# Optimization experiments

Hardware: AMD Instinct MI355X
Metric: run time of the kernel (lower is better)

The kernel has to match this reference:

```python
import jax, jax.numpy as jnp
import numpy as np

KERNEL_SIZE = 6
PAD = (KERNEL_SIZE - 2) // 4  # 1


def _polyphase(k1d):
    # torch: flip(k.reshape(-1,2).permute(1,0), dims=(1,)) -> (2, K/2)
    # row 0 = even-index taps reversed, row 1 = odd-index taps reversed
    return jnp.flip(k1d.reshape(-1, 2).T, axis=1)


def _upfir_last(x, f):
    """Polyphase synthesis along last axis.
    x: (..., N), f: (2, K2). Pads reflect by PAD, correlates with each
    polyphase filter (stride-1 cross-correlation as in F.conv2d), then
    interleaves the two outputs -> (..., 2N). Even outputs come from f[0].
    """
    N = x.shape[-1]
    K2 = f.shape[1]
    pad_cfg = [(0, 0)] * (x.ndim - 1) + [(PAD, PAD)]
    xp = jnp.pad(x, pad_cfg, mode='reflect')  # (..., N + 2*PAD), N+2*PAD-K2+1 == N
    y0 = sum(f[0, j] * xp[..., j:j + N] for j in range(K2))
    y1 = sum(f[1, j] * xp[..., j:j + N] for j in range(K2))
    return jnp.stack([y0, y1], axis=-1).reshape(*x.shape[:-1], 2 * N)


def _upfir_rows(x, f):
    # synthesis along axis -2 (the H axis); matches torch's .mT transpose dance
    return jnp.swapaxes(_upfir_last(jnp.swapaxes(x, -1, -2), f), -1, -2)


def setup_inputs() -> dict:
    key = jax.random.key(0)
    ks = jax.random.split(key, 6)
    B, C, H, W = 4, 64, 256, 256
    return {
        'ss': jax.random.normal(ks[0], (B, C, H, W), dtype=jnp.float32),
        'sd': jax.random.normal(ks[1], (B, C, H, W), dtype=jnp.float32),
        'ds': jax.random.normal(ks[2], (B, C, H, W), dtype=jnp.float32),
        'dd': jax.random.normal(ks[3], (B, C, H, W), dtype=jnp.float32),
        'h': jax.random.normal(ks[4], (KERNEL_SIZE,), dtype=jnp.float32),
        'g': jax.random.normal(ks[5], (KERNEL_SIZE,), dtype=jnp.float32),
    }


def reference(ss, sd, ds, dd, h, g):
    # single level inverse 2D DWT (levels=1, normalize_approximation=False)
    fh = _polyphase(h)
    fg = _polyphase(g)
    # columns pass (along H): reconstruct low-pass rows `s` and high-pass rows `d`
    s = _upfir_rows(ss, fh) + _upfir_rows(sd, fg)  # (B,C,2H,W)
    d = _upfir_rows(ds, fh) + _upfir_rows(dd, fg)  # (B,C,2H,W)
    # rows pass (along W)
    out = _upfir_last(s, fh) + _upfir_last(d, fg)  # (B,C,2H,2W)
    return out
```

## Files before the change

### kernel.cpp

```cpp
#include <hip/hip_runtime.h>


typedef float float4v __attribute__((ext_vector_type(4)));

constexpr int Hc = 256;
constexpr int Wc = 256;
constexpr int ROWS = 8;
constexpr int WPB  = 4;

__global__ __launch_bounds__(256) void idwt_kernel(
    const float* __restrict__ ss, const float* __restrict__ sd,
    const float* __restrict__ ds, const float* __restrict__ dd,
    const float* __restrict__ hf, const float* __restrict__ gf,
    float* __restrict__ out)
{
    const int lane = threadIdx.x;
    const int wid  = threadIdx.y;
    const int i0   = (blockIdx.x * WPB + wid) * ROWS;
    const int bc   = blockIdx.y;

    const float h0 = hf[0], h1 = hf[1], h2 = hf[2];
    const float h3 = hf[3], h4 = hf[4], h5 = hf[5];
    const float g0 = gf[0], g1 = gf[1], g2 = gf[2];
    const float g3 = gf[3], g4 = gf[4], g5 = gf[5];

    const size_t off = (size_t)bc * (Hc * Wc);
    const int j0 = lane * 4;
    const float* pss = ss + off + j0;
    const float* psd = sd + off + j0;
    const float* pds = ds + off + j0;
    const float* pdd = dd + off + j0;

    auto ld = [&](const float* p, int r) -> float4v {
        return *reinterpret_cast<const float4v*>(p + (size_t)r * Wc);
    };

    const int rm = (i0 == 0) ? 1 : i0 - 1;
    float4v s_m = ld(pss, rm), s_c = ld(pss, i0);
    float4v t_m = ld(psd, rm), t_c = ld(psd, i0);
    float4v u_m = ld(pds, rm), u_c = ld(pds, i0);
    float4v v_m = ld(pdd, rm), v_c = ld(pdd, i0);

    const int W2 = 2 * Wc;
    float* obase = out + (size_t)bc * (2 * Hc) * W2 + 8 * lane;

    auto left = [&](const float4v& w) -> float {
        float l = __shfl_up(w[3], 1);
        return (lane == 0) ? w[1] : l;
    };
    auto right = [&](const float4v& w) -> float {
        float rr = __shfl_down(w[0], 1);
        return (lane == 63) ? w[2] : rr;
    };

    #pragma unroll
    for (int r = 0; r < ROWS; ++r) {
        const int i  = i0 + r;
        const int rn = (i + 1 < Hc) ? i + 1 : Hc - 2;
        const float4v s_p = ld(pss, rn);
        const float4v t_p = ld(psd, rn);
        const float4v u_p = ld(pds, rn);
        const float4v v_p = ld(pdd, rn);

        float4v vs0, vs1, vd0, vd1;
        #pragma unroll
        for (int k = 0; k < 4; ++k) {
            vs0[k] = h4*s_m[k] + h2*s_c[k] + h0*s_p[k] + g4*t_m[k] + g2*t_c[k] + g0*t_p[k];
            vs1[k] = h5*s_m[k] + h3*s_c[k] + h1*s_p[k] + g5*t_m[k] + g3*t_c[k] + g1*t_p[k];
            vd0[k] = h4*u_m[k] + h2*u_c[k] + h0*u_p[k] + g4*v_m[k] + g2*v_c[k] + g0*v_p[k];
            vd1[k] = h5*u_m[k] + h3*u_c[k] + h1*u_p[k] + g5*v_m[k] + g3*v_c[k] + g1*v_p[k];
        }

        const float a [6] = { left(vs0), vs0[0], vs0[1], vs0[2], vs0[3], right(vs0) };
        const float b [6] = { left(vd0), vd0[0], vd0[1], vd0[2], vd0[3], right(vd0) };
        const float c2[6] = { left(vs1), vs1[0], vs1[1], vs1[2], vs1[3], right(vs1) };
        const float d2[6] = { left(vd1), vd1[0], vd1[1], vd1[2], vd1[3], right(vd1) };

        float4v o00, o01, o10, o11;
        #pragma unroll
        for (int t = 0; t < 4; ++t) {
            const float e0 = h4*a [t] + h2*a [t+1] + h0*a [t+2] + g4*b [t] + g2*b [t+1] + g0*b [t+2];
            const float e1 = h5*a [t] + h3*a [t+1] + h1*a [t+2] + g5*b [t] + g3*b [t+1] + g1*b [t+2];
            const float f0 = h4*c2[t] + h2*c2[t+1] + h0*c2[t+2] + g4*d2[t] + g2*d2[t+1] + g0*d2[t+2];
            const float f1 = h5*c2[t] + h3*c2[t+1] + h1*c2[t+2] + g5*d2[t] + g3*d2[t+1] + g1*d2[t+2];
            if (t < 2) {
                o00[2*t]   = e0; o00[2*t+1]     = e1;
                o10[2*t]   = f0; o10[2*t+1]     = f1;
            } else {
                o01[2*(t-2)]   = e0; o01[2*(t-2)+1] = e1;
                o11[2*(t-2)]   = f0; o11[2*(t-2)+1] = f1;
            }
        }

        float* orow0 = obase + (size_t)(2 * i) * W2;
        float* orow1 = orow0 + W2;
        *reinterpret_cast<float4v*>(orow0)     = o00;
        *reinterpret_cast<float4v*>(orow0 + 4) = o01;
        *reinterpret_cast<float4v*>(orow1)     = o10;
        *reinterpret_cast<float4v*>(orow1 + 4) = o11;

        s_m = s_c; s_c = s_p;
        t_m = t_c; t_c = t_p;
        u_m = u_c; u_c = u_p;
        v_m = v_c; v_c = v_p;
    }
}

extern "C" void kernel_launch(void* const* d_in, const int* in_sizes, int n_in,
                              void* d_out, int out_size, void* d_ws, size_t ws_size,
                              hipStream_t stream) {
    const float* ss = (const float*)d_in[0];
    const float* sd = (const float*)d_in[1];
    const float* ds = (const float*)d_in[2];
    const float* dd = (const float*)d_in[3];
    const float* hf = (const float*)d_in[4];
    const float* gf = (const float*)d_in[5];
    float* out = (float*)d_out;

    const int BC = in_sizes[0] / (Hc * Wc);
    dim3 block(64, WPB);
    dim3 grid(Hc / (ROWS * WPB), BC);
    idwt_kernel<<<grid, block, 0, stream>>>(ss, sd, ds, dd, hf, gf, out);
}
```

Baseline: 452.8 us.

## Split each row across two wavefronts with seam column recompute

Each wavefront now covers half a row (128 columns, two per lane) instead of a full row (four per lane). Blocks pair two column tiles with two row strips, so the grid doubles and there are twice as many waves to hide memory latency. The boundary column at the seam between tiles is loaded redundantly and its vertical filter recomputed so that no cross-wave communication is needed. The trade-off is extra scalar loads per row and narrower vector loads and stores.

```diff
diff --git a/kernel.cpp b/kernel.cpp
--- a/kernel.cpp
+++ b/kernel.cpp
@@ -1,12 +1,13 @@
 #include <hip/hip_runtime.h>
 
 
+typedef float float2v __attribute__((ext_vector_type(2)));
 typedef float float4v __attribute__((ext_vector_type(4)));
 
 constexpr int Hc = 256;
 constexpr int Wc = 256;
 constexpr int ROWS = 8;
-constexpr int WPB  = 4;
+constexpr int TW   = 128;
 
 __global__ __launch_bounds__(256) void idwt_kernel(
     const float* __restrict__ ss, const float* __restrict__ sd,
@@ -15,8 +16,10 @@
     float* __restrict__ out)
 {
     const int lane = threadIdx.x;
-    const int wid  = threadIdx.y;
-    const int i0   = (blockIdx.x * WPB + wid) * ROWS;
+    const int wv   = threadIdx.y;
+    const int tile = wv & 1;
+    const int rs   = wv >> 1;
+    const int i0   = (blockIdx.x * 2 + rs) * ROWS;
     const int bc   = blockIdx.y;
 
     const float h0 = hf[0], h1 = hf[1], h2 = hf[2];
@@ -25,84 +28,90 @@
     const float g3 = gf[3], g4 = gf[4], g5 = gf[5];
 
     const size_t off = (size_t)bc * (Hc * Wc);
-    const int j0 = lane * 4;
-    const float* pss = ss + off + j0;
-    const float* psd = sd + off + j0;
-    const float* pds = ds + off + j0;
-    const float* pdd = dd + off + j0;
+    const int c0 = tile * TW + 2 * lane;
+    const float* pss = ss + off;
+    const float* psd = sd + off;
+    const float* pds = ds + off;
+    const float* pdd = dd + off;
 
-    auto ld = [&](const float* p, int r) -> float4v {
-        return *reinterpret_cast<const float4v*>(p + (size_t)r * Wc);
+    auto ld2 = [&](const float* p, int r) -> float2v {
+        return *reinterpret_cast<const float2v*>(p + (size_t)r * Wc + c0);
+    };
+    const int seam = tile ? (TW - 1) : TW;
+    auto lde = [&](const float* p, int r) -> float {
+        return p[(size_t)r * Wc + seam];
     };
 
     const int rm = (i0 == 0) ? 1 : i0 - 1;
-    float4v s_m = ld(pss, rm), s_c = ld(pss, i0);
-    float4v t_m = ld(psd, rm), t_c = ld(psd, i0);
-    float4v u_m = ld(pds, rm), u_c = ld(pds, i0);
-    float4v v_m = ld(pdd, rm), v_c = ld(pdd, i0);
+    float2v s_m = ld2(pss, rm), s_c = ld2(pss, i0);
+    float2v t_m = ld2(psd, rm), t_c = ld2(psd, i0);
+    float2v u_m = ld2(pds, rm), u_c = ld2(pds, i0);
+    float2v v_m = ld2(pdd, rm), v_c = ld2(pdd, i0);
+    float es_m = lde(pss, rm), es_c = lde(pss, i0);
+    float et_m = lde(psd, rm), et_c = lde(psd, i0);
+    float eu_m = lde(pds, rm), eu_c = lde(pds, i0);
+    float ev_m = lde(pdd, rm), ev_c = lde(pdd, i0);
 
     const int W2 = 2 * Wc;
-    float* obase = out + (size_t)bc * (2 * Hc) * W2 + 8 * lane;
-
-    auto left = [&](const float4v& w) -> float {
-        float l = __shfl_up(w[3], 1);
-        return (lane == 0) ? w[1] : l;
-    };
-    auto right = [&](const float4v& w) -> float {
-        float rr = __shfl_down(w[0], 1);
-        return (lane == 63) ? w[2] : rr;
-    };
+    float* obase = out + (size_t)bc * (2 * Hc) * W2 + tile * (2 * TW) + 4 * lane;
 
     #pragma unroll
     for (int r = 0; r < ROWS; ++r) {
         const int i  = i0 + r;
         const int rn = (i + 1 < Hc) ? i + 1 : Hc - 2;
-        const float4v s_p = ld(pss, rn);
-        const float4v t_p = ld(psd, rn);
-        const float4v u_p = ld(pds, rn);
-        const float4v v_p = ld(pdd, rn);
+        const float2v s_p = ld2(pss, rn);
+        const float2v t_p = ld2(psd, rn);
+        const float2v u_p = ld2(pds, rn);
+        const float2v v_p = ld2(pdd, rn);
+        const float es_p = lde(pss, rn);
+        const float et_p = lde(psd, rn);
+        const float eu_p = lde(pds, rn);
+        const float ev_p = lde(pdd, rn);
 
-        float4v vs0, vs1, vd0, vd1;
+        float2v vs0, vs1, vd0, vd1;
         #pragma unroll
-        for (int k = 0; k < 4; ++k) {
+        for (int k = 0; k < 2; ++k) {
             vs0[k] = h4*s_m[k] + h2*s_c[k] + h0*s_p[k] + g4*t_m[k] + g2*t_c[k] + g0*t_p[k];
             vs1[k] = h5*s_m[k] + h3*s_c[k] + h1*s_p[k] + g5*t_m[k] + g3*t_c[k] + g1*t_p[k];
             vd0[k] = h4*u_m[k] + h2*u_c[k] + h0*u_p[k] + g4*v_m[k] + g2*v_c[k] + g0*v_p[k];
             vd1[k] = h5*u_m[k] + h3*u_c[k] + h1*u_p[k] + g5*v_m[k] + g3*v_c[k] + g1*v_p[k];
         }
+        const float sS0 = h4*es_m + h2*es_c + h0*es_p + g4*et_m + g2*et_c + g0*et_p;
+        const float sS1 = h5*es_m + h3*es_c + h1*es_p + g5*et_m + g3*et_c + g1*et_p;
+        const float sD0 = h4*eu_m + h2*eu_c + h0*eu_p + g4*ev_m + g2*ev_c + g0*ev_p;
+        const float sD1 = h5*eu_m + h3*eu_c + h1*eu_p + g5*ev_m + g3*ev_c + g1*ev_p;
 
-        const float a [6] = { left(vs0), vs0[0], vs0[1], vs0[2], vs0[3], right(vs0) };
-        const float b [6] = { left(vd0), vd0[0], vd0[1], vd0[2], vd0[3], right(vd0) };
-        const float c2[6] = { left(vs1), vs1[0], vs1[1], vs1[2], vs1[3], right(vs1) };
-        const float d2[6] = { left(vd1), vd1[0], vd1[1], vd1[2], vd1[3], right(vd1) };
+        auto lnb = [&](const float2v& v, float sv) -> float {
+            float x = __shfl_up(v[1], 1);
+            return (lane == 0) ? (tile ? sv : v[1]) : x;
+        };
+        auto rnb = [&](const float2v& v, float sv) -> float {
+            float x = __shfl_down(v[0], 1);
+            return (lane == 63) ? (tile ? v[0] : sv) : x;
+        };
+        const float La = lnb(vs0, sS0), Ra = rnb(vs0, sS0);
+        const float Lb = lnb(vd0, sD0), Rb = rnb(vd0, sD0);
+        const float Lc = lnb(vs1, sS1), Rc = rnb(vs1, sS1);
+        const float Ld = lnb(vd1, sD1), Rd = rnb(vd1, sD1);
 
-        float4v o00, o01, o10, o11;
-        #pragma unroll
-        for (int t = 0; t < 4; ++t) {
-            const float e0 = h4*a [t] + h2*a [t+1] + h0*a [t+2] + g4*b [t] + g2*b [t+1] + g0*b [t+2];
-            const float e1 = h5*a [t] + h3*a [t+1] + h1*a [t+2] + g5*b [t] + g3*b [t+1] + g1*b [t+2];
-            const float f0 = h4*c2[t] + h2*c2[t+1] + h0*c2[t+2] + g4*d2[t] + g2*d2[t+1] + g0*d2[t+2];
-            const float f1 = h5*c2[t] + h3*c2[t+1] + h1*c2[t+2] + g5*d2[t] + g3*d2[t+1] + g1*d2[t+2];
-            if (t < 2) {
-                o00[2*t]   = e0; o00[2*t+1]     = e1;
-                o10[2*t]   = f0; o10[2*t+1]     = f1;
-            } else {
-                o01[2*(t-2)]   = e0; o01[2*(t-2)+1] = e1;
-                o11[2*(t-2)]   = f0; o11[2*(t-2)+1] = f1;
-            }
-        }
+        float4v o0, o1;
+        o0[0] = h4*La      + h2*vs0[0] + h0*vs0[1] + g4*Lb      + g2*vd0[0] + g0*vd0[1];
+        o0[1] = h5*La      + h3*vs0[0] + h1*vs0[1] + g5*Lb      + g3*vd0[0] + g1*vd0[1];
+        o0[2] = h4*vs0[0]  + h2*vs0[1] + h0*Ra     + g4*vd0[0]  + g2*vd0[1] + g0*Rb;
+        o0[3] = h5*vs0[0]  + h3*vs0[1] + h1*Ra     + g5*vd0[0]  + g3*vd0[1] + g1*Rb;
+        o1[0] = h4*Lc      + h2*vs1[0] + h0*vs1[1] + g4*Ld      + g2*vd1[0] + g0*vd1[1];
+        o1[1] = h5*Lc      + h3*vs1[0] + h1*vs1[1] + g5*Ld      + g3*vd1[0] + g1*vd1[1];
+        o1[2] = h4*vs1[0]  + h2*vs1[1] + h0*Rc     + g4*vd1[0]  + g2*vd1[1] + g0*Rd;
+        o1[3] = h5*vs1[0]  + h3*vs1[1] + h1*Rc     + g5*vd1[0]  + g3*vd1[1] + g1*Rd;
 
         float* orow0 = obase + (size_t)(2 * i) * W2;
-        float* orow1 = orow0 + W2;
-        *reinterpret_cast<float4v*>(orow0)     = o00;
-        *reinterpret_cast<float4v*>(orow0 + 4) = o01;
-        *reinterpret_cast<float4v*>(orow1)     = o10;
-        *reinterpret_cast<float4v*>(orow1 + 4) = o11;
+        *reinterpret_cast<float4v*>(orow0)      = o0;
+        *reinterpret_cast<float4v*>(orow0 + W2) = o1;
 
-        s_m = s_c; s_c = s_p;
-        t_m = t_c; t_c = t_p;
-        u_m = u_c; u_c = u_p;
-        v_m = v_c; v_c = v_p;
+        s_m = s_c; s_c = s_p;  t_m = t_c; t_c = t_p;
+        u_m = u_c; u_c = u_p;  v_m = v_c; v_c = v_p;
+        es_m = es_c; es_c = es_p;  et_m = et_c; et_c = et_p;
+        eu_m = eu_c; eu_c = eu_p;  ev_m = ev_c; ev_c = ev_p;
     }
 }
 
@@ -118,7 +127,7 @@
     float* out = (float*)d_out;
 
     const int BC = in_sizes[0] / (Hc * Wc);
-    dim3 block(64, WPB);
-    dim3 grid(Hc / (ROWS * WPB), BC);
+    dim3 block(64, 4);
+    dim3 grid(Hc / (ROWS * 2), BC);
     idwt_kernel<<<grid, block, 0, stream>>>(ss, sd, ds, dd, hf, gf, out);
 }
```

Measured after the change: 450.7 us. Within noise of the previous version (-0.5%).
